# Performance work log

Measured on AMD Instinct MI355X. Metric: run time of the kernel, lower is better.

## Reference

```python
import jax, jax.numpy as jnp
import numpy as np

B, HW, C = 32, 56, 128
WS, SS, NH = 7, 3, 4
HD = C // NH
SCALE = HD ** -0.5
NWIN = (HW // WS) ** 2  # 64 windows per image
N = WS * WS             # 49 tokens per window


def _build_constants():
    # relative position index [N, N] into flattened (13*13) bias table
    coords = np.stack(np.meshgrid(np.arange(WS), np.arange(WS), indexing='ij'))  # [2,7,7]
    cf = coords.reshape(2, -1)                       # [2,49]
    rel = cf[:, :, None] - cf[:, None, :]            # [2,49,49]
    rel = rel.transpose(1, 2, 0).copy()              # [49,49,2]
    rel[:, :, 0] += WS - 1
    rel[:, :, 1] += WS - 1
    rel[:, :, 0] *= 2 * WS - 1
    pos_index = rel.sum(-1)                          # [49,49]
    # shifted-window attention mask [nW, N, N]
    img = np.zeros((HW, HW))
    sl = (slice(0, -WS), slice(-WS, -SS), slice(-SS, None))
    cnt = 0
    for h in sl:
        for w in sl:
            img[h, w] = cnt
            cnt += 1
    mw = img.reshape(HW // WS, WS, HW // WS, WS).transpose(0, 2, 1, 3).reshape(NWIN, N)
    am = mw[:, None, :] - mw[:, :, None]             # unsqueeze(1) - unsqueeze(2)
    am = np.where(am != 0, -100.0, 0.0).astype(np.float32)
    return jnp.asarray(pos_index), jnp.asarray(am)

POS_INDEX, ATTN_MASK = _build_constants()


def _ln(x, w, b, eps=1e-5):
    mu = x.mean(-1, keepdims=True)
    var = ((x - mu) ** 2).mean(-1, keepdims=True)
    return (x - mu) * jax.lax.rsqrt(var + eps) * w + b


def setup_inputs() -> dict:
    key = jax.random.key(0)
    ks = jax.random.split(key, 10)
    s = 0.02
    return {
        'x': jax.random.normal(ks[0], (B, HW * HW, C), jnp.float32),
        'norm1_w': jnp.ones((C,), jnp.float32),
        'norm1_b': jnp.zeros((C,), jnp.float32),
        'qkv_w': jax.random.normal(ks[1], (C, 3 * C), jnp.float32) * s,
        'qkv_b': jax.random.normal(ks[2], (3 * C,), jnp.float32) * s,
        'proj_w': jax.random.normal(ks[3], (C, C), jnp.float32) * s,
        'proj_b': jax.random.normal(ks[4], (C,), jnp.float32) * s,
        'pos_bias_table': jax.random.normal(ks[5], (2 * WS - 1, 2 * WS - 1, NH), jnp.float32) * s,
        'mlp_w1': jax.random.normal(ks[6], (C, 4 * C), jnp.float32) * s,
        'mlp_b1': jnp.zeros((4 * C,), jnp.float32),
        'mlp_w2': jax.random.normal(ks[7], (4 * C, C), jnp.float32) * s,
        'mlp_b2': jnp.zeros((C,), jnp.float32),
        'norm2_w': jnp.ones((C,), jnp.float32),
        'norm2_b': jnp.zeros((C,), jnp.float32),
    }


def reference(x, norm1_w, norm1_b, qkv_w, qkv_b, proj_w, proj_b, pos_bias_table,
              mlp_w1, mlp_b1, mlp_w2, mlp_b2, norm2_w, norm2_b):
    G = HW // WS  # grid of windows per side
    Bw = B * NWIN
    shortcut = x
    y = _ln(x, norm1_w, norm1_b).reshape(B, HW, HW, C)
    # cyclic shift
    y = jnp.roll(y, (-SS, -SS), axis=(1, 2))
    # window partition -> [B*nW, 49, C]
    yw = y.reshape(B, G, WS, G, WS, C).transpose(0, 1, 3, 2, 4, 5).reshape(Bw, N, C)
    # qkv projection
    qkv = (yw @ qkv_w + qkv_b).reshape(Bw, N, 3, NH, HD).transpose(2, 0, 3, 1, 4)
    q, k, v = qkv[0] * SCALE, qkv[1], qkv[2]  # [Bw, NH, N, HD]
    attn = jnp.einsum('bhnd,bhmd->bhnm', q, k)
    # relative position bias [NH, N, N]
    bias = pos_bias_table.reshape(-1, NH)[POS_INDEX]  # [N,N,NH]
    attn = attn + bias.transpose(2, 0, 1)[None]
    # shift mask per window
    attn = attn.reshape(B, NWIN, NH, N, N) + ATTN_MASK[None, :, None]
    attn = jax.nn.softmax(attn.reshape(Bw, NH, N, N), axis=-1)
    out = jnp.einsum('bhnm,bhmd->bhnd', attn, v).transpose(0, 2, 1, 3).reshape(Bw, N, C)
    out = out @ proj_w + proj_b
    # window reverse
    out = out.reshape(B, G, G, WS, WS, C).transpose(0, 1, 3, 2, 4, 5).reshape(B, HW, HW, C)
    out = jnp.roll(out, (SS, SS), axis=(1, 2)).reshape(B, HW * HW, C)
    x = shortcut + out
    h = _ln(x, norm2_w, norm2_b)
    h = jax.nn.gelu(h @ mlp_w1 + mlp_b1, approximate=False) @ mlp_w2 + mlp_b2
    return x + h
```

## Files before the change

kernel.cpp:

```cpp
#include <hip/hip_runtime.h>
#include <hip/hip_bf16.h>

#define NTOK 100352
#define SCALE_Q 0.17677669529663687f

typedef __bf16 bf16x8 __attribute__((ext_vector_type(8)));
typedef float f32x4 __attribute__((ext_vector_type(4)));
struct bf2 { __hip_bfloat16 x, y; };
struct __align__(8) bh4 { __hip_bfloat16 a, b, c, d; };

__device__ __forceinline__ int wt_to_tok(int wt) {
  int w = wt / 49, n = wt - w * 49;
  int b = w >> 6, wi = w & 63;
  int gh = wi >> 3, gw = wi & 7;
  int r = n / 7, c = n - r * 7;
  int hs = gh * 7 + r + 3; if (hs >= 56) hs -= 56;
  int ws = gw * 7 + c + 3; if (ws >= 56) ws -= 56;
  return (b * 56 + hs) * 56 + ws;
}

__device__ __forceinline__ float gelu_fast(float v) {
  float y = 0.7978845608028654f * (v + 0.044715f * v * v * v);
  float ay = fabsf(y);
  float e = __expf(-2.0f * ay);
  float t = (1.0f - e) / (1.0f + e);
  t = copysignf(t, y);
  return 0.5f * v * (1.0f + t);
}

__global__ __launch_bounds__(256) void prep_all(const float* __restrict__ qkvw,
                                                const float* __restrict__ projw,
                                                const float* __restrict__ w1,
                                                const float* __restrict__ w2,
                                                __hip_bfloat16* __restrict__ dst) {
  int i = blockIdx.x * 256 + threadIdx.x;
  float v;
  if (i < 49152) { int n = i >> 7, k = i & 127; v = qkvw[k * 384 + n]; }
  else if (i < 65536) { int j = i - 49152; int n = j >> 7, k = j & 127; v = projw[k * 128 + n]; }
  else if (i < 131072) { int j = i - 65536; int n = j >> 7, k = j & 127; v = w1[k * 512 + n]; }
  else { int j = i - 131072; int n = j / 512, k = j - n * 512; v = w2[k * 128 + n]; }
  dst[i] = __float2bfloat16(v);
}

__global__ __launch_bounds__(256) void ln1_apply(const float* __restrict__ x,
                                                 const float* __restrict__ nw,
                                                 const float* __restrict__ nb,
                                                 __hip_bfloat16* __restrict__ xn) {
  int wt = blockIdx.x * 4 + (threadIdx.x >> 6);
  int lane = threadIdx.x & 63;
  int tok = wt_to_tok(wt);
  float2 v = *(const float2*)(x + (size_t)tok * 128 + lane * 2);
  float s = v.x + v.y, ss = v.x * v.x + v.y * v.y;
#pragma unroll
  for (int off = 32; off; off >>= 1) {
    s += __shfl_xor(s, off);
    ss += __shfl_xor(ss, off);
  }
  float mu = s * (1.0f / 128.0f);
  float rstd = rsqrtf(ss * (1.0f / 128.0f) - mu * mu + 1e-5f);
  float2 wv = *(const float2*)(nw + lane * 2);
  float2 bv = *(const float2*)(nb + lane * 2);
  bf2 o;
  o.x = __float2bfloat16((v.x - mu) * rstd * wv.x + bv.x);
  o.y = __float2bfloat16((v.y - mu) * rstd * wv.y + bv.y);
  *(bf2*)(xn + (size_t)wt * 128 + lane * 2) = o;
}

__global__ __launch_bounds__(256) void attn_mfma(const __hip_bfloat16* __restrict__ qkv,
                                                 const float* __restrict__ ptab,
                                                 __hip_bfloat16* __restrict__ attnout) {
  __shared__ __align__(16) char lds[4 * 12288];
  const int tid = threadIdx.x;
  const int lane = tid & 63, h = tid >> 6;
  const int w = blockIdx.x;
  const int wi = w & 63, gh = wi >> 3, gw = wi & 7;
  char* Pl = lds + h * 12288;
  char* VTl = Pl + 8192;
  const int lxi = lane & 15, lq = lane >> 4, lg4 = (lane >> 4) * 4;

  const __hip_bfloat16* base = qkv + (size_t)w * 49 * 384 + h * 32;
  __hip_bfloat16* op = attnout + (size_t)w * 49 * 128 + h * 32;

  bf16x8 qa[4], kb[4];
#pragma unroll
  for (int mi = 0; mi < 4; ++mi) {
    int t = mi * 16 + lxi; if (t > 48) t = 48;
    qa[mi] = *(const bf16x8*)(base + (size_t)t * 384 + lq * 8);
    kb[mi] = *(const bf16x8*)(base + (size_t)t * 384 + 128 + lq * 8);
  }
  {
    union { bf16x8 v; __hip_bfloat16 e[8]; } vv[4];
    const __hip_bfloat16* vp = base + (size_t)(lane < 49 ? lane : 0) * 384 + 256;
#pragma unroll
    for (int q = 0; q < 4; ++q) vv[q].v = *(const bf16x8*)(vp + q * 8);
    __hip_bfloat16 z = __float2bfloat16(0.0f);
#pragma unroll
    for (int q = 0; q < 4; ++q)
#pragma unroll
      for (int e = 0; e < 8; ++e) {
        int d = q * 8 + e;
        __hip_bfloat16 val = (lane < 49) ? vv[q].e[e] : z;
        *(__hip_bfloat16*)(VTl + d * 128 + ((lane * 2) ^ ((d & 7) << 4))) = val;
      }
  }

  f32x4 s[4][4] = {};
#pragma unroll
  for (int mi = 0; mi < 4; ++mi)
#pragma unroll
    for (int ni = 0; ni < 4; ++ni)
      s[mi][ni] = __builtin_amdgcn_mfma_f32_16x16x32_bf16(qa[mi], kb[ni], s[mi][ni], 0, 0, 0);

  int rj[4], cj[4], cntj[4], jbad[4];
#pragma unroll
  for (int ni = 0; ni < 4; ++ni) {
    int jc = ni * 16 + lxi;
    jbad[ni] = (jc > 48);
    int jj = jbad[ni] ? 48 : jc;
    rj[ni] = jj / 7; cj[ni] = jj - rj[ni] * 7;
    int hj = gh * 7 + rj[ni], wj = gw * 7 + cj[ni];
    cntj[ni] = (hj < 49 ? 0 : (hj < 53 ? 3 : 6)) + (wj < 49 ? 0 : (wj < 53 ? 1 : 2));
  }
#pragma unroll
  for (int mi = 0; mi < 4; ++mi)
#pragma unroll
    for (int j = 0; j < 4; ++j) {
      int i = mi * 16 + lg4 + j; if (i > 48) i = 48;
      int ri = i / 7, ci = i - ri * 7;
      int hi_ = gh * 7 + ri, wi_ = gw * 7 + ci;
      int cnti = (hi_ < 49 ? 0 : (hi_ < 53 ? 3 : 6)) + (wi_ < 49 ? 0 : (wi_ < 53 ? 1 : 2));
#pragma unroll
      for (int ni = 0; ni < 4; ++ni) {
        float b = ptab[((ri - rj[ni] + 6) * 13 + (ci - cj[ni] + 6)) * 4 + h];
        float val = s[mi][ni][j] * SCALE_Q + b;
        if (cnti != cntj[ni]) val -= 100.0f;
        if (jbad[ni]) val = -1e30f;
        s[mi][ni][j] = val;
      }
    }

#pragma unroll
  for (int mi = 0; mi < 4; ++mi)
#pragma unroll
    for (int j = 0; j < 4; ++j) {
      float m = fmaxf(fmaxf(s[mi][0][j], s[mi][1][j]), fmaxf(s[mi][2][j], s[mi][3][j]));
#pragma unroll
      for (int off = 8; off; off >>= 1) m = fmaxf(m, __shfl_xor(m, off));
      float e[4], sum = 0.0f;
#pragma unroll
      for (int ni = 0; ni < 4; ++ni) { e[ni] = __expf(s[mi][ni][j] - m); sum += e[ni]; }
#pragma unroll
      for (int off = 8; off; off >>= 1) sum += __shfl_xor(sum, off);
      float inv = 1.0f / sum;
#pragma unroll
      for (int ni = 0; ni < 4; ++ni) s[mi][ni][j] = e[ni] * inv;
    }

#pragma unroll
  for (int mi = 0; mi < 4; ++mi)
#pragma unroll
    for (int j = 0; j < 4; ++j) {
      int row = mi * 16 + lg4 + j;
      int sw = (row & 7) << 4;
      char* prow = Pl + row * 128;
#pragma unroll
      for (int ni = 0; ni < 4; ++ni)
        *(__hip_bfloat16*)(prow + (((ni * 16 + lxi) * 2) ^ sw)) =
            __float2bfloat16(s[mi][ni][j]);
    }

  __syncthreads();

  f32x4 o[4][2] = {};
#pragma unroll
  for (int ks = 0; ks < 2; ++ks) {
    bf16x8 pa[4], vb[2];
#pragma unroll
    for (int mi = 0; mi < 4; ++mi) {
      int row = mi * 16 + lxi;
      pa[mi] = *(const bf16x8*)(Pl + row * 128 + ((ks * 64 + lq * 16) ^ ((row & 7) << 4)));
    }
#pragma unroll
    for (int ni = 0; ni < 2; ++ni) {
      int row = ni * 16 + lxi;
      vb[ni] = *(const bf16x8*)(VTl + row * 128 + ((ks * 64 + lq * 16) ^ ((row & 7) << 4)));
    }
#pragma unroll
    for (int mi = 0; mi < 4; ++mi)
#pragma unroll
      for (int ni = 0; ni < 2; ++ni)
        o[mi][ni] = __builtin_amdgcn_mfma_f32_16x16x32_bf16(pa[mi], vb[ni], o[mi][ni], 0, 0, 0);
  }

#pragma unroll
  for (int mi = 0; mi < 4; ++mi)
#pragma unroll
    for (int j = 0; j < 4; ++j) {
      int q = mi * 16 + lg4 + j;
      if (q < 49) {
#pragma unroll
        for (int ni = 0; ni < 2; ++ni)
          op[(size_t)q * 128 + ni * 16 + lxi] = __float2bfloat16(o[mi][ni][j]);
      }
    }
}

template<int EPI>
__global__ __launch_bounds__(256) void gemm_mfma(
    const __hip_bfloat16* __restrict__ A, int lda, int NB,
    const __hip_bfloat16* __restrict__ Wt,
    const float* __restrict__ bias,
    void* __restrict__ outv, int ldo,
    __hip_bfloat16* __restrict__ out2,
    const float* __restrict__ nw, const float* __restrict__ nb,
    const float* __restrict__ resf)
{
  __shared__ float redS[256], redQ[256];
  const int bid = blockIdx.x;
  const int xcd = bid & 7, tt = bid >> 3;
  const int nbk = tt % NB, mseq = tt / NB;
  const int m0 = (mseq * 8 + xcd) * 128, n0 = nbk * 128;
  const int tid = threadIdx.x;
  const int lane = tid & 63, wid = tid >> 6;
  const int wm = wid >> 1, wn = wid & 1;
  const int lrow = lane & 15, lq = lane >> 4;

  f32x4 acc[4][4] = {};

  const __hip_bfloat16* arow[4];
  const __hip_bfloat16* brow[4];
#pragma unroll
  for (int mi = 0; mi < 4; ++mi)
    arow[mi] = A + (size_t)(m0 + wm * 64 + mi * 16 + lrow) * lda + lq * 8;
#pragma unroll
  for (int ni = 0; ni < 4; ++ni)
    brow[ni] = Wt + (size_t)(n0 + wn * 64 + ni * 16 + lrow) * 128 + lq * 8;

#pragma unroll
  for (int ks = 0; ks < 4; ++ks) {
    bf16x8 af[4], bfr[4];
#pragma unroll
    for (int mi = 0; mi < 4; ++mi) af[mi] = *(const bf16x8*)(arow[mi] + ks * 32);
#pragma unroll
    for (int ni = 0; ni < 4; ++ni) bfr[ni] = *(const bf16x8*)(brow[ni] + ks * 32);
#pragma unroll
    for (int mi = 0; mi < 4; ++mi)
#pragma unroll
      for (int ni = 0; ni < 4; ++ni)
        acc[mi][ni] = __builtin_amdgcn_mfma_f32_16x16x32_bf16(af[mi], bfr[ni], acc[mi][ni], 0, 0, 0);
  }

  float bv[4];
#pragma unroll
  for (int ni = 0; ni < 4; ++ni) bv[ni] = bias[n0 + wn * 64 + ni * 16 + lrow];

  if (EPI == 4) {
    __hip_bfloat16* x2 = (__hip_bfloat16*)outv;
    float nwc[4], nbc[4];
#pragma unroll
    for (int ni = 0; ni < 4; ++ni) {
      int colg = wn * 64 + ni * 16 + lrow;
      nwc[ni] = nw[colg]; nbc[ni] = nb[colg];
    }
    int toks[4][4];
#pragma unroll
    for (int mi = 0; mi < 4; ++mi)
#pragma unroll
      for (int j = 0; j < 4; ++j) {
        int row = wm * 64 + mi * 16 + lq * 4 + j;
        int tok = wt_to_tok(m0 + row);
        toks[mi][j] = tok;
        float s = 0.0f, ss = 0.0f;
#pragma unroll
        for (int ni = 0; ni < 4; ++ni) {
          int colg = wn * 64 + ni * 16 + lrow;
          float val = acc[mi][ni][j] + bv[ni] + resf[(size_t)tok * 128 + colg];
          x2[(size_t)tok * 128 + colg] = __float2bfloat16(val);
          acc[mi][ni][j] = val;
          s += val; ss += val * val;
        }
#pragma unroll
        for (int off = 8; off; off >>= 1) {
          s += __shfl_xor(s, off);
          ss += __shfl_xor(ss, off);
        }
        if (lrow == 0) { redS[row * 2 + wn] = s; redQ[row * 2 + wn] = ss; }
      }
    __syncthreads();
#pragma unroll
    for (int mi = 0; mi < 4; ++mi)
#pragma unroll
      for (int j = 0; j < 4; ++j) {
        int row = wm * 64 + mi * 16 + lq * 4 + j;
        float s = redS[row * 2] + redS[row * 2 + 1];
        float ss = redQ[row * 2] + redQ[row * 2 + 1];
        float mu = s * (1.0f / 128.0f);
        float rstd = rsqrtf(ss * (1.0f / 128.0f) - mu * mu + 1e-5f);
        int tok = toks[mi][j];
#pragma unroll
        for (int ni = 0; ni < 4; ++ni) {
          int colg = wn * 64 + ni * 16 + lrow;
          float xnv = (acc[mi][ni][j] - mu) * rstd * nwc[ni] + nbc[ni];
          out2[(size_t)tok * 128 + colg] = __float2bfloat16(xnv);
        }
      }
    return;
  }

#pragma unroll
  for (int mi = 0; mi < 4; ++mi) {
#pragma unroll
    for (int j = 0; j < 4; ++j) {
      int rowg = m0 + wm * 64 + mi * 16 + lq * 4 + j;
#pragma unroll
      for (int ni = 0; ni < 4; ++ni) {
        int colg = n0 + wn * 64 + ni * 16 + lrow;
        float val = acc[mi][ni][j] + bv[ni];
        ((__hip_bfloat16*)outv)[(size_t)rowg * ldo + colg] = __float2bfloat16(val);
      }
    }
  }
}

__global__ __launch_bounds__(256) void mlp_fused(
    const __hip_bfloat16* __restrict__ x2n,
    const __hip_bfloat16* __restrict__ w1T,
    const float* __restrict__ b1,
    const __hip_bfloat16* __restrict__ w2T,
    const float* __restrict__ b2,
    const __hip_bfloat16* __restrict__ x2,
    float* __restrict__ out)
{
  __shared__ __align__(16) char Hs[2][64 * 256];
  const int m0 = blockIdx.x * 64;
  const int tid = threadIdx.x;
  const int lane = tid & 63, wid = tid >> 6;
  const int wh = wid >> 1, wv = wid & 1;
  const int lrow = lane & 15, lq = lane >> 4;

  f32x4 oacc[2][4] = {};

  for (int c = 0; c < 4; ++c) {
    f32x4 hacc[4][2] = {};
#pragma unroll
    for (int ks = 0; ks < 4; ++ks) {
      bf16x8 wf[4], afr[2];
#pragma unroll
      for (int mi = 0; mi < 4; ++mi) {
        int hd = c * 128 + wh * 64 + mi * 16 + lrow;
        wf[mi] = *(const bf16x8*)(w1T + (size_t)hd * 128 + ks * 32 + lq * 8);
      }
#pragma unroll
      for (int ni = 0; ni < 2; ++ni) {
        int r = m0 + wv * 32 + ni * 16 + lrow;
        afr[ni] = *(const bf16x8*)(x2n + (size_t)r * 128 + ks * 32 + lq * 8);
      }
#pragma unroll
      for (int mi = 0; mi < 4; ++mi)
#pragma unroll
        for (int ni = 0; ni < 2; ++ni)
          hacc[mi][ni] = __builtin_amdgcn_mfma_f32_16x16x32_bf16(wf[mi], afr[ni], hacc[mi][ni], 0, 0, 0);
    }
    char* hbuf = Hs[c & 1];
#pragma unroll
    for (int mi = 0; mi < 4; ++mi) {
      int hdb = wh * 64 + mi * 16 + lq * 4;
      float b1v[4];
#pragma unroll
      for (int j = 0; j < 4; ++j) b1v[j] = b1[c * 128 + hdb + j];
#pragma unroll
      for (int ni = 0; ni < 2; ++ni) {
        int m_ = wv * 32 + ni * 16 + lrow;
        bh4 hv;
        hv.a = __float2bfloat16(gelu_fast(hacc[mi][ni][0] + b1v[0]));
        hv.b = __float2bfloat16(gelu_fast(hacc[mi][ni][1] + b1v[1]));
        hv.c = __float2bfloat16(gelu_fast(hacc[mi][ni][2] + b1v[2]));
        hv.d = __float2bfloat16(gelu_fast(hacc[mi][ni][3] + b1v[3]));
        *(bh4*)(hbuf + m_ * 256 + ((hdb * 2) ^ ((m_ & 7) << 4))) = hv;
      }
    }
    __syncthreads();
#pragma unroll
    for (int ks = 0; ks < 4; ++ks) {
      int kb = ks * 64 + lq * 16;
      bf16x8 hf[2], w2f[4];
#pragma unroll
      for (int mi = 0; mi < 2; ++mi) {
        int r = wh * 32 + mi * 16 + lrow;
        hf[mi] = *(const bf16x8*)(hbuf + r * 256 + (kb ^ ((r & 7) << 4)));
      }
#pragma unroll
      for (int ni = 0; ni < 4; ++ni) {
        int n = wv * 64 + ni * 16 + lrow;
        w2f[ni] = *(const bf16x8*)(w2T + (size_t)n * 512 + c * 128 + ks * 32 + lq * 8);
      }
#pragma unroll
      for (int mi = 0; mi < 2; ++mi)
#pragma unroll
        for (int ni = 0; ni < 4; ++ni)
          oacc[mi][ni] = __builtin_amdgcn_mfma_f32_16x16x32_bf16(hf[mi], w2f[ni], oacc[mi][ni], 0, 0, 0);
    }
  }

  float bv[4];
#pragma unroll
  for (int ni = 0; ni < 4; ++ni) bv[ni] = b2[wv * 64 + ni * 16 + lrow];
#pragma unroll
  for (int mi = 0; mi < 2; ++mi)
#pragma unroll
    for (int j = 0; j < 4; ++j) {
      int row = m0 + wh * 32 + mi * 16 + lq * 4 + j;
#pragma unroll
      for (int ni = 0; ni < 4; ++ni) {
        int col = wv * 64 + ni * 16 + lrow;
        float r = __bfloat162float(x2[(size_t)row * 128 + col]);
        out[(size_t)row * 128 + col] = oacc[mi][ni][j] + bv[ni] + r;
      }
    }
}

extern "C" void kernel_launch(void* const* d_in, const int* in_sizes, int n_in,
                              void* d_out, int out_size, void* d_ws, size_t ws_size,
                              hipStream_t stream) {
  (void)in_sizes; (void)n_in; (void)out_size; (void)ws_size;
  const float* x     = (const float*)d_in[0];
  const float* n1w   = (const float*)d_in[1];
  const float* n1b   = (const float*)d_in[2];
  const float* qkvw  = (const float*)d_in[3];
  const float* qkvb  = (const float*)d_in[4];
  const float* projw = (const float*)d_in[5];
  const float* projb = (const float*)d_in[6];
  const float* ptab  = (const float*)d_in[7];
  const float* w1    = (const float*)d_in[8];
  const float* b1    = (const float*)d_in[9];
  const float* w2    = (const float*)d_in[10];
  const float* b2    = (const float*)d_in[11];
  const float* n2w   = (const float*)d_in[12];
  const float* n2b   = (const float*)d_in[13];
  float* out = (float*)d_out;

  char* ws = (char*)d_ws;
  __hip_bfloat16* xn      = (__hip_bfloat16*)ws;
  __hip_bfloat16* qkv     = (__hip_bfloat16*)(ws + 25690112);
  __hip_bfloat16* attnout = (__hip_bfloat16*)(ws + 102760448);
  __hip_bfloat16* x2      = (__hip_bfloat16*)(ws + 128450560);
  __hip_bfloat16* x2n     = (__hip_bfloat16*)(ws + 154140672);
  __hip_bfloat16* wbase   = (__hip_bfloat16*)(ws + 179830784);
  __hip_bfloat16* qkvwT  = wbase;
  __hip_bfloat16* projwT = wbase + 49152;
  __hip_bfloat16* w1T    = wbase + 65536;
  __hip_bfloat16* w2T    = wbase + 131072;

  prep_all<<<768, 256, 0, stream>>>(qkvw, projw, w1, w2, wbase);
  ln1_apply<<<NTOK / 4, 256, 0, stream>>>(x, n1w, n1b, xn);
  gemm_mfma<0><<<784 * 3, 256, 0, stream>>>(xn, 128, 3, qkvwT, qkvb,
                                            qkv, 384, nullptr, nullptr, nullptr,
                                            nullptr);
  attn_mfma<<<2048, 256, 0, stream>>>(qkv, ptab, attnout);
  gemm_mfma<4><<<784, 256, 0, stream>>>(attnout, 128, 1, projwT, projb,
                                        x2, 128, x2n, n2w, n2b, x);
  mlp_fused<<<1568, 256, 0, stream>>>(x2n, w1T, b1, w2T, b2, x2, out);
}
```

Measured before the change: 292.6 us.

## Restructure fused MLP to 32-row tiles with full hidden layer in LDS

The fused MLP kernel now processes 32 tokens per block instead of 64. Each of the four waves computes a 128-wide slice of the 512 hidden units in one pass and writes the GELU output into a 32x512 LDS buffer. After a single barrier, each wave produces 32 output columns over the full K=512. This drops the four-chunk loop and its per-chunk barriers and doubles the grid size. In exchange, w1/w2 weight reads from global memory double per token and per-wave MFMA reuse is lower.

```diff
diff --git a/kernel.cpp b/kernel.cpp
--- a/kernel.cpp
+++ b/kernel.cpp
@@ -331,88 +331,79 @@
     const __hip_bfloat16* __restrict__ x2,
     float* __restrict__ out)
 {
-  __shared__ __align__(16) char Hs[2][64 * 256];
-  const int m0 = blockIdx.x * 64;
+  __shared__ __align__(16) char Hs[32 * 1024];
+  const int m0 = blockIdx.x * 32;
   const int tid = threadIdx.x;
-  const int lane = tid & 63, wid = tid >> 6;
-  const int wh = wid >> 1, wv = wid & 1;
-  const int lrow = lane & 15, lq = lane >> 4;
-
-  f32x4 oacc[2][4] = {};
-
-  for (int c = 0; c < 4; ++c) {
-    f32x4 hacc[4][2] = {};
-#pragma unroll
-    for (int ks = 0; ks < 4; ++ks) {
-      bf16x8 wf[4], afr[2];
-#pragma unroll
-      for (int mi = 0; mi < 4; ++mi) {
-        int hd = c * 128 + wh * 64 + mi * 16 + lrow;
-        wf[mi] = *(const bf16x8*)(w1T + (size_t)hd * 128 + ks * 32 + lq * 8);
-      }
+  const int lane = tid & 63, w = tid >> 6;
+  const int lrow = lane & 15, lq = lane >> 4, lg4 = (lane >> 4) * 4;
+
+  f32x4 hacc[8][2] = {};
+#pragma unroll
+  for (int ks = 0; ks < 4; ++ks) {
+    bf16x8 afr[2], wf[8];
+#pragma unroll
+    for (int ni = 0; ni < 2; ++ni)
+      afr[ni] = *(const bf16x8*)(x2n + (size_t)(m0 + ni * 16 + lrow) * 128 + ks * 32 + lq * 8);
+#pragma unroll
+    for (int mi = 0; mi < 8; ++mi)
+      wf[mi] = *(const bf16x8*)(w1T + (size_t)(w * 128 + mi * 16 + lrow) * 128 + ks * 32 + lq * 8);
+#pragma unroll
+    for (int mi = 0; mi < 8; ++mi)
+#pragma unroll
+      for (int ni = 0; ni < 2; ++ni)
+        hacc[mi][ni] = __builtin_amdgcn_mfma_f32_16x16x32_bf16(wf[mi], afr[ni], hacc[mi][ni], 0, 0, 0);
+  }
+
+#pragma unroll
+  for (int mi = 0; mi < 8; ++mi) {
+    int hd0 = w * 128 + mi * 16 + lg4;
+    float b1v[4];
+#pragma unroll
+    for (int j = 0; j < 4; ++j) b1v[j] = b1[hd0 + j];
+#pragma unroll
+    for (int ni = 0; ni < 2; ++ni) {
+      int m_ = ni * 16 + lrow;
+      bh4 hv;
+      hv.a = __float2bfloat16(gelu_fast(hacc[mi][ni][0] + b1v[0]));
+      hv.b = __float2bfloat16(gelu_fast(hacc[mi][ni][1] + b1v[1]));
+      hv.c = __float2bfloat16(gelu_fast(hacc[mi][ni][2] + b1v[2]));
+      hv.d = __float2bfloat16(gelu_fast(hacc[mi][ni][3] + b1v[3]));
+      *(bh4*)(Hs + m_ * 1024 + ((hd0 * 2) ^ ((m_ & 7) << 4))) = hv;
+    }
+  }
+
+  __syncthreads();
+
+  f32x4 oacc[2][2] = {};
+#pragma unroll
+  for (int ks = 0; ks < 16; ++ks) {
+    bf16x8 hf[2], w2f[2];
+#pragma unroll
+    for (int mi = 0; mi < 2; ++mi) {
+      int r = mi * 16 + lrow;
+      hf[mi] = *(const bf16x8*)(Hs + r * 1024 + ((ks * 64 + lq * 16) ^ ((r & 7) << 4)));
+    }
+#pragma unroll
+    for (int ni = 0; ni < 2; ++ni)
+      w2f[ni] = *(const bf16x8*)(w2T + (size_t)(w * 32 + ni * 16 + lrow) * 512 + ks * 32 + lq * 8);
+#pragma unroll
+    for (int mi = 0; mi < 2; ++mi)
+#pragma unroll
+      for (int ni = 0; ni < 2; ++ni)
+        oacc[mi][ni] = __builtin_amdgcn_mfma_f32_16x16x32_bf16(hf[mi], w2f[ni], oacc[mi][ni], 0, 0, 0);
+  }
+
+  float bv[2];
+#pragma unroll
+  for (int ni = 0; ni < 2; ++ni) bv[ni] = b2[w * 32 + ni * 16 + lrow];
+#pragma unroll
+  for (int mi = 0; mi < 2; ++mi)
+#pragma unroll
+    for (int j = 0; j < 4; ++j) {
+      int row = m0 + mi * 16 + lg4 + j;
 #pragma unroll
       for (int ni = 0; ni < 2; ++ni) {
-        int r = m0 + wv * 32 + ni * 16 + lrow;
-        afr[ni] = *(const bf16x8*)(x2n + (size_t)r * 128 + ks * 32 + lq * 8);
-      }
-#pragma unroll
-      for (int mi = 0; mi < 4; ++mi)
-#pragma unroll
-        for (int ni = 0; ni < 2; ++ni)
-          hacc[mi][ni] = __builtin_amdgcn_mfma_f32_16x16x32_bf16(wf[mi], afr[ni], hacc[mi][ni], 0, 0, 0);
-    }
-    char* hbuf = Hs[c & 1];
-#pragma unroll
-    for (int mi = 0; mi < 4; ++mi) {
-      int hdb = wh * 64 + mi * 16 + lq * 4;
-      float b1v[4];
-#pragma unroll
-      for (int j = 0; j < 4; ++j) b1v[j] = b1[c * 128 + hdb + j];
-#pragma unroll
-      for (int ni = 0; ni < 2; ++ni) {
-        int m_ = wv * 32 + ni * 16 + lrow;
-        bh4 hv;
-        hv.a = __float2bfloat16(gelu_fast(hacc[mi][ni][0] + b1v[0]));
-        hv.b = __float2bfloat16(gelu_fast(hacc[mi][ni][1] + b1v[1]));
-        hv.c = __float2bfloat16(gelu_fast(hacc[mi][ni][2] + b1v[2]));
-        hv.d = __float2bfloat16(gelu_fast(hacc[mi][ni][3] + b1v[3]));
-        *(bh4*)(hbuf + m_ * 256 + ((hdb * 2) ^ ((m_ & 7) << 4))) = hv;
-      }
-    }
-    __syncthreads();
-#pragma unroll
-    for (int ks = 0; ks < 4; ++ks) {
-      int kb = ks * 64 + lq * 16;
-      bf16x8 hf[2], w2f[4];
-#pragma unroll
-      for (int mi = 0; mi < 2; ++mi) {
-        int r = wh * 32 + mi * 16 + lrow;
-        hf[mi] = *(const bf16x8*)(hbuf + r * 256 + (kb ^ ((r & 7) << 4)));
-      }
-#pragma unroll
-      for (int ni = 0; ni < 4; ++ni) {
-        int n = wv * 64 + ni * 16 + lrow;
-        w2f[ni] = *(const bf16x8*)(w2T + (size_t)n * 512 + c * 128 + ks * 32 + lq * 8);
-      }
-#pragma unroll
-      for (int mi = 0; mi < 2; ++mi)
-#pragma unroll
-        for (int ni = 0; ni < 4; ++ni)
-          oacc[mi][ni] = __builtin_amdgcn_mfma_f32_16x16x32_bf16(hf[mi], w2f[ni], oacc[mi][ni], 0, 0, 0);
-    }
-  }
-
-  float bv[4];
-#pragma unroll
-  for (int ni = 0; ni < 4; ++ni) bv[ni] = b2[wv * 64 + ni * 16 + lrow];
-#pragma unroll
-  for (int mi = 0; mi < 2; ++mi)
-#pragma unroll
-    for (int j = 0; j < 4; ++j) {
-      int row = m0 + wh * 32 + mi * 16 + lq * 4 + j;
-#pragma unroll
-      for (int ni = 0; ni < 4; ++ni) {
-        int col = wv * 64 + ni * 16 + lrow;
+        int col = w * 32 + ni * 16 + lrow;
         float r = __bfloat162float(x2[(size_t)row * 128 + col]);
         out[(size_t)row * 128 + col] = oacc[mi][ni][j] + bv[ni] + r;
       }
@@ -459,5 +450,5 @@
   attn_mfma<<<2048, 256, 0, stream>>>(qkv, ptab, attnout);
   gemm_mfma<4><<<784, 256, 0, stream>>>(attnout, 128, 1, projwT, projb,
                                         x2, 128, x2n, n2w, n2b, x);
-  mlp_fused<<<1568, 256, 0, stream>>>(x2n, w1T, b1, w2T, b2, x2, out);
-}
+  mlp_fused<<<3136, 256, 0, stream>>>(x2n, w1T, b1, w2T, b2, x2, out);
+}
```

After: 273.9 us. 6.4% less time.
